# Kernel optimization log

Measured on AMD Instinct MI355X. Metric: run time of the kernel, lower is better.

## Reference

```python
import jax, jax.numpy as jnp
import numpy as np

N = 100000          # nodes
E = 1600000         # edges (before self-loops)
F_IN = 256          # num_node_features
F_MID = F_IN // 2   # conv1 out = 128
HID = 128           # hidden_channels
OUT = 64            # num_label_features
G = 128             # num graphs in batch
NEG_SLOPE = 0.2


def setup_inputs() -> dict:
    key = jax.random.key(0)
    ks = jax.random.split(key, 16)
    s = 0.05
    return {
        "x": jax.random.normal(ks[0], (N, F_IN), dtype=jnp.float32),
        "edge_index": jax.random.randint(ks[1], (2, E), 0, N, dtype=jnp.int64),
        "batch": jnp.sort(jax.random.randint(ks[2], (N,), 0, G, dtype=jnp.int64)),
        # GATConv 1 (heads=1)
        "W1": jax.random.normal(ks[3], (F_IN, F_MID), jnp.float32) * s,
        "a1_src": jax.random.normal(ks[4], (F_MID,), jnp.float32) * s,
        "a1_dst": jax.random.normal(ks[5], (F_MID,), jnp.float32) * s,
        "b1": jnp.zeros((F_MID,), jnp.float32),
        # GATConv 2
        "W2": jax.random.normal(ks[6], (F_MID, HID), jnp.float32) * s,
        "a2_src": jax.random.normal(ks[7], (HID,), jnp.float32) * s,
        "a2_dst": jax.random.normal(ks[8], (HID,), jnp.float32) * s,
        "b2": jnp.zeros((HID,), jnp.float32),
        # GlobalAttention gate nn
        "gate_W": jax.random.normal(ks[9], (HID, 1), jnp.float32) * s,
        "gate_b": jnp.zeros((1,), jnp.float32),
        # final linear
        "lin_W": jax.random.normal(ks[10], (HID, OUT), jnp.float32) * s,
        "lin_b": jnp.zeros((OUT,), jnp.float32),
    }


def _gat_conv(x, edge_index, W, a_src, a_dst, bias):
    """PyG GATConv, heads=1, add_self_loops=True, negative_slope=0.2."""
    n = x.shape[0]
    h = x @ W                                   # [N, F]
    loop = jnp.arange(n, dtype=edge_index.dtype)
    src = jnp.concatenate([edge_index[0], loop])  # message sources j
    dst = jnp.concatenate([edge_index[1], loop])  # aggregation targets i
    # per-node attention logits, gathered per-edge
    al = (h @ a_src)[src] + (h @ a_dst)[dst]    # [E+N]
    al = jax.nn.leaky_relu(al, NEG_SLOPE)
    # segment softmax over incoming edges of each dst node
    m = jax.ops.segment_max(al, dst, num_segments=n)
    e = jnp.exp(al - m[dst])
    s = jax.ops.segment_sum(e, dst, num_segments=n)
    coef = e / (s[dst] + 1e-16)
    out = jax.ops.segment_sum(h[src] * coef[:, None], dst, num_segments=n)
    return out + bias


def reference(x, edge_index, batch, W1, a1_src, a1_dst, b1,
              W2, a2_src, a2_dst, b2, gate_W, gate_b, lin_W, lin_b):
    h = _gat_conv(x, edge_index, W1, a1_src, a1_dst, b1)
    h = jax.nn.relu(h)
    h = _gat_conv(h, edge_index, W2, a2_src, a2_dst, b2)
    # GlobalAttention pooling: segment softmax of gate over batch ids
    gate = (h @ gate_W + gate_b)[:, 0]          # [N]
    gm = jax.ops.segment_max(gate, batch, num_segments=G)
    ge = jnp.exp(gate - gm[batch])
    gs = jax.ops.segment_sum(ge, batch, num_segments=G)
    attn = ge / (gs[batch] + 1e-16)
    pooled = jax.ops.segment_sum(h * attn[:, None], batch, num_segments=G)  # [G, HID]
    pooled = jax.nn.relu(pooled)
    # dropout p=0.5 is identity at inference
    return pooled @ lin_W + lin_b               # [G, OUT]
```

## Files before the change

### kernel.cpp

```cpp
#include <hip/hip_runtime.h>
#include <hip/hip_bf16.h>
#include <math.h>

#define NNODES 100000
#define NEDGES 1600000
#define EN     1700000
#define F_IN   256
#define F_MID  128
#define HID    128
#define NG     128
#define NOUT   64
#define SCAN_CHUNK 2048
#define NCHUNK ((NNODES + SCAN_CHUNK - 1) / SCAN_CHUNK)

typedef unsigned int  u32;
typedef unsigned short u16;

__device__ __forceinline__ float bfl(u32 u) { return __uint_as_float(u << 16); }
__device__ __forceinline__ float bfh(u32 u) { return __uint_as_float(u & 0xFFFF0000u); }
__device__ __forceinline__ u32 f2bf(float f) {
    u32 x = __float_as_uint(f);
    return (x + 0x7FFFu + ((x >> 16) & 1u)) >> 16;
}

__global__ __launch_bounds__(256) void k_init(int* deg, float* gs, float* pooled) {
    int i = blockIdx.x * 256 + threadIdx.x;
    if (i < NNODES) deg[i] = 1;
    if (i < NG) gs[i] = 0.f;
    if (i < NG * HID) pooled[i] = 0.f;
}

__global__ __launch_bounds__(256) void k_count(const int* __restrict__ ei, int* deg) {
    int e = blockIdx.x * 256 + threadIdx.x;
    if (e >= NEDGES) return;
    atomicAdd(&deg[ei[NEDGES + e]], 1);
}

__global__ __launch_bounds__(256) void k_scan_chunk(const int* __restrict__ deg,
                                                    int* rowptr, int* part) {
    __shared__ int sums[256];
    int c = blockIdx.x, t = threadIdx.x;
    int base = c * SCAN_CHUNK;
    int v[8]; int s = 0;
#pragma unroll
    for (int i = 0; i < 8; i++) {
        int idx = base + t * 8 + i;
        v[i] = (idx < NNODES) ? deg[idx] : 0;
        s += v[i];
    }
    sums[t] = s;
    __syncthreads();
    for (int off = 1; off < 256; off <<= 1) {
        int x = (t >= off) ? sums[t - off] : 0;
        __syncthreads();
        sums[t] += x;
        __syncthreads();
    }
    int run = (t == 0) ? 0 : sums[t - 1];
#pragma unroll
    for (int i = 0; i < 8; i++) {
        int idx = base + t * 8 + i;
        if (idx < NNODES) rowptr[idx] = run;
        run += v[i];
    }
    if (t == 255) part[c] = sums[255];
}

__global__ void k_scan_part(int* part, int nc) {
    if (threadIdx.x == 0) {
        int run = 0;
        for (int c = 0; c < nc; c++) { int v = part[c]; part[c] = run; run += v; }
    }
}

__global__ __launch_bounds__(256) void k_scan_add(int* rowptr, int* cursor,
                                                  const int* __restrict__ part) {
    int i = blockIdx.x * 256 + threadIdx.x;
    if (i >= NNODES) return;
    int v = rowptr[i] + part[i >> 11];
    rowptr[i] = v;
    cursor[i] = v;
}

__global__ __launch_bounds__(256) void k_fill(const int* __restrict__ ei,
                                              int* cursor, int* srcs) {
    int e = blockIdx.x * 256 + threadIdx.x;
    if (e >= EN) return;
    int src, dst;
    if (e < NEDGES) { src = ei[e]; dst = ei[NEDGES + e]; }
    else            { src = dst = e - NEDGES; }
    int pos = atomicAdd(&cursor[dst], 1);
    srcs[pos] = src;
}

template <int K, bool ABF>
__global__ __launch_bounds__(256) void k_gemm(const void* __restrict__ Av,
                                              const float* __restrict__ B,
                                              u16* __restrict__ C, int M) {
    __shared__ float As[16][128];
    __shared__ float Bs[16][128];
    int bm = blockIdx.x * 128;
    int tid = threadIdx.x;
    int tx = tid & 15, ty = tid >> 4;
    float acc[8][8] = {};
    for (int k0 = 0; k0 < K; k0 += 16) {
#pragma unroll
        for (int q = tid; q < 512; q += 256) {
            int m = q >> 2, kq = (q & 3) << 2;
            int row = bm + m;
            if (ABF) {
                const u16* A = (const u16*)Av;
                uint2 v = make_uint2(0u, 0u);
                if (row < M) v = *(const uint2*)(A + (size_t)row * K + k0 + kq);
                As[kq + 0][m] = bfl(v.x); As[kq + 1][m] = bfh(v.x);
                As[kq + 2][m] = bfl(v.y); As[kq + 3][m] = bfh(v.y);
            } else {
                const float* A = (const float*)Av;
                float4 v = make_float4(0.f, 0.f, 0.f, 0.f);
                if (row < M) v = *(const float4*)(A + (size_t)row * K + k0 + kq);
                As[kq + 0][m] = v.x; As[kq + 1][m] = v.y;
                As[kq + 2][m] = v.z; As[kq + 3][m] = v.w;
            }
        }
#pragma unroll
        for (int q = tid; q < 512; q += 256) {
            int kk = q >> 5, n4 = (q & 31) << 2;
            *(float4*)(&Bs[kk][n4]) = *(const float4*)(B + (size_t)(k0 + kk) * 128 + n4);
        }
        __syncthreads();
#pragma unroll
        for (int kk = 0; kk < 16; kk++) {
            float a[8], b[8];
            *(float4*)(a)     = *(float4*)(&As[kk][ty * 8]);
            *(float4*)(a + 4) = *(float4*)(&As[kk][ty * 8 + 4]);
            *(float4*)(b)     = *(float4*)(&Bs[kk][tx * 8]);
            *(float4*)(b + 4) = *(float4*)(&Bs[kk][tx * 8 + 4]);
#pragma unroll
            for (int i = 0; i < 8; i++)
#pragma unroll
                for (int j = 0; j < 8; j++)
                    acc[i][j] = fmaf(a[i], b[j], acc[i][j]);
        }
        __syncthreads();
    }
#pragma unroll
    for (int i = 0; i < 8; i++) {
        int row = bm + ty * 8 + i;
        if (row < M) {
            uint4 o;
            o.x = f2bf(acc[i][0]) | (f2bf(acc[i][1]) << 16);
            o.y = f2bf(acc[i][2]) | (f2bf(acc[i][3]) << 16);
            o.z = f2bf(acc[i][4]) | (f2bf(acc[i][5]) << 16);
            o.w = f2bf(acc[i][6]) | (f2bf(acc[i][7]) << 16);
            *(uint4*)(C + (size_t)row * 128 + tx * 8) = o;
        }
    }
}

__global__ __launch_bounds__(256) void k_dots(const u32* __restrict__ h,
                                              const float* __restrict__ asrc,
                                              const float* __restrict__ adst,
                                              float* as_, float* ad_) {
    int wid = (blockIdx.x * 256 + threadIdx.x) >> 6;
    int lane = threadIdx.x & 63;
    if (wid >= NNODES) return;
    u32 u = h[(size_t)wid * 64 + lane];
    float vx = bfl(u), vy = bfh(u);
    float2 as2 = ((const float2*)asrc)[lane];
    float2 ad2 = ((const float2*)adst)[lane];
    float s = vx * as2.x + vy * as2.y;
    float d = vx * ad2.x + vy * ad2.y;
#pragma unroll
    for (int off = 32; off; off >>= 1) {
        s += __shfl_xor(s, off);
        d += __shfl_xor(d, off);
    }
    if (lane == 0) { as_[wid] = s; ad_[wid] = d; }
}

template <bool RELU, bool GATE, bool OUTBF>
__global__ __launch_bounds__(256) void k_agg(
    const u32* __restrict__ h, const float* __restrict__ as_,
    const float* __restrict__ ad_, const int* __restrict__ rowptr,
    const int* __restrict__ rowend, const int* __restrict__ srcs,
    const float* __restrict__ bias, void* __restrict__ outv,
    const float* __restrict__ gateW, const float* __restrict__ gateB,
    float* __restrict__ gatev, float* __restrict__ gs,
    const int* __restrict__ batch) {
    int wid = (blockIdx.x * 256 + threadIdx.x) >> 6;
    int lane = threadIdx.x & 63;
    if (wid >= NNODES) return;
    int row = rowptr[wid];
    int dg = rowend[wid] - row;
    float adn = ad_[wid];

    float ssum = 0.f;
    float2 a0 = {0.f, 0.f}, a1 = {0.f, 0.f}, a2 = {0.f, 0.f}, a3 = {0.f, 0.f};
    float2 a4 = {0.f, 0.f}, a5 = {0.f, 0.f}, a6 = {0.f, 0.f}, a7 = {0.f, 0.f};

    for (int base = 0; base < dg; base += 64) {
        int k = base + lane;
        float ev = 0.f; int sk = 0;
        if (k < dg) {
            sk = srcs[row + k];
            float al = as_[sk] + adn;
            al = (al > 0.f) ? al : 0.2f * al;
            ev = __expf(al);
            ssum += ev;
        }
        int rem = dg - base; if (rem > 64) rem = 64;
        int kk = 0;
        for (; kk + 8 <= rem; kk += 8) {
            int   s0 = __shfl(sk, kk + 0), s1 = __shfl(sk, kk + 1);
            int   s2 = __shfl(sk, kk + 2), s3 = __shfl(sk, kk + 3);
            int   s4 = __shfl(sk, kk + 4), s5 = __shfl(sk, kk + 5);
            int   s6 = __shfl(sk, kk + 6), s7 = __shfl(sk, kk + 7);
            float e0 = __shfl(ev, kk + 0), e1 = __shfl(ev, kk + 1);
            float e2 = __shfl(ev, kk + 2), e3 = __shfl(ev, kk + 3);
            float e4 = __shfl(ev, kk + 4), e5 = __shfl(ev, kk + 5);
            float e6 = __shfl(ev, kk + 6), e7 = __shfl(ev, kk + 7);
            u32 u0 = h[(size_t)s0 * 64 + lane];
            u32 u1 = h[(size_t)s1 * 64 + lane];
            u32 u2 = h[(size_t)s2 * 64 + lane];
            u32 u3 = h[(size_t)s3 * 64 + lane];
            u32 u4 = h[(size_t)s4 * 64 + lane];
            u32 u5 = h[(size_t)s5 * 64 + lane];
            u32 u6 = h[(size_t)s6 * 64 + lane];
            u32 u7 = h[(size_t)s7 * 64 + lane];
            a0.x = fmaf(e0, bfl(u0), a0.x); a0.y = fmaf(e0, bfh(u0), a0.y);
            a1.x = fmaf(e1, bfl(u1), a1.x); a1.y = fmaf(e1, bfh(u1), a1.y);
            a2.x = fmaf(e2, bfl(u2), a2.x); a2.y = fmaf(e2, bfh(u2), a2.y);
            a3.x = fmaf(e3, bfl(u3), a3.x); a3.y = fmaf(e3, bfh(u3), a3.y);
            a4.x = fmaf(e4, bfl(u4), a4.x); a4.y = fmaf(e4, bfh(u4), a4.y);
            a5.x = fmaf(e5, bfl(u5), a5.x); a5.y = fmaf(e5, bfh(u5), a5.y);
            a6.x = fmaf(e6, bfl(u6), a6.x); a6.y = fmaf(e6, bfh(u6), a6.y);
            a7.x = fmaf(e7, bfl(u7), a7.x); a7.y = fmaf(e7, bfh(u7), a7.y);
        }
        for (; kk + 2 <= rem; kk += 2) {
            int   s0 = __shfl(sk, kk + 0), s1 = __shfl(sk, kk + 1);
            float e0 = __shfl(ev, kk + 0), e1 = __shfl(ev, kk + 1);
            u32 u0 = h[(size_t)s0 * 64 + lane];
            u32 u1 = h[(size_t)s1 * 64 + lane];
            a0.x = fmaf(e0, bfl(u0), a0.x); a0.y = fmaf(e0, bfh(u0), a0.y);
            a1.x = fmaf(e1, bfl(u1), a1.x); a1.y = fmaf(e1, bfh(u1), a1.y);
        }
        if (kk < rem) {
            int   s0 = __shfl(sk, kk);
            float e0 = __shfl(ev, kk);
            u32 u0 = h[(size_t)s0 * 64 + lane];
            a0.x = fmaf(e0, bfl(u0), a0.x); a0.y = fmaf(e0, bfh(u0), a0.y);
        }
    }
    float2 acc;
    acc.x = ((a0.x + a1.x) + (a2.x + a3.x)) + ((a4.x + a5.x) + (a6.x + a7.x));
    acc.y = ((a0.y + a1.y) + (a2.y + a3.y)) + ((a4.y + a5.y) + (a6.y + a7.y));
#pragma unroll
    for (int off = 32; off; off >>= 1) ssum += __shfl_xor(ssum, off);
    float inv = 1.f / (ssum + 1e-16f);
    float2 b2v = ((const float2*)bias)[lane];
    float o0 = acc.x * inv + b2v.x;
    float o1 = acc.y * inv + b2v.y;
    if (RELU) { o0 = fmaxf(o0, 0.f); o1 = fmaxf(o1, 0.f); }
    if (OUTBF) {
        ((u32*)outv)[(size_t)wid * 64 + lane] = f2bf(o0) | (f2bf(o1) << 16);
    } else {
        ((float2*)((float*)outv + (size_t)wid * 128))[lane] = make_float2(o0, o1);
    }
    if (GATE) {
        float2 gw = ((const float2*)gateW)[lane];
        float g = o0 * gw.x + o1 * gw.y;
#pragma unroll
        for (int off = 32; off; off >>= 1) g += __shfl_xor(g, off);
        if (lane == 0) {
            float ge = __expf(g + gateB[0]);
            gatev[wid] = ge;
            atomicAdd(&gs[batch[wid]], ge);
        }
    }
}

__global__ __launch_bounds__(128) void k_pool(const float* __restrict__ h,
                                              const float* __restrict__ gatev,
                                              const float* __restrict__ gs,
                                              const int* __restrict__ batch,
                                              float* pooled) {
    int t = threadIdx.x;
    int chunk = (NNODES + gridDim.x - 1) / gridDim.x;
    int s0 = blockIdx.x * chunk;
    int s1 = s0 + chunk; if (s1 > NNODES) s1 = NNODES;
    if (s0 >= s1) return;
    int curg = batch[s0];
    float invs = 1.f / (gs[curg] + 1e-16f);
    float acc = 0.f;
    for (int i = s0; i < s1; i++) {
        int g = batch[i];
        if (g != curg) {
            atomicAdd(&pooled[curg * 128 + t], acc);
            acc = 0.f; curg = g;
            invs = 1.f / (gs[g] + 1e-16f);
        }
        acc += h[(size_t)i * 128 + t] * (gatev[i] * invs);
    }
    atomicAdd(&pooled[curg * 128 + t], acc);
}

__global__ __launch_bounds__(64) void k_final(const float* __restrict__ pooled,
                                              const float* __restrict__ linW,
                                              const float* __restrict__ linb,
                                              float* __restrict__ out) {
    __shared__ float rowv[128];
    int g = blockIdx.x, t = threadIdx.x;
    rowv[t]      = fmaxf(pooled[g * 128 + t], 0.f);
    rowv[t + 64] = fmaxf(pooled[g * 128 + 64 + t], 0.f);
    __syncthreads();
    float acc = linb[t];
#pragma unroll 8
    for (int k = 0; k < 128; k++) acc = fmaf(rowv[k], linW[k * 64 + t], acc);
    out[g * 64 + t] = acc;
}

extern "C" void kernel_launch(void* const* d_in, const int* in_sizes, int n_in,
                              void* d_out, int out_size, void* d_ws, size_t ws_size,
                              hipStream_t stream) {
    const float* x     = (const float*)d_in[0];
    const int*   ei    = (const int*)d_in[1];
    const int*   batch = (const int*)d_in[2];
    const float* W1    = (const float*)d_in[3];
    const float* a1s   = (const float*)d_in[4];
    const float* a1d   = (const float*)d_in[5];
    const float* b1    = (const float*)d_in[6];
    const float* W2    = (const float*)d_in[7];
    const float* a2s   = (const float*)d_in[8];
    const float* a2d   = (const float*)d_in[9];
    const float* b2    = (const float*)d_in[10];
    const float* gateW = (const float*)d_in[11];
    const float* gateB = (const float*)d_in[12];
    const float* linW  = (const float*)d_in[13];
    const float* linb  = (const float*)d_in[14];
    float* out = (float*)d_out;

    char* p = (char*)d_ws;
    auto alloc = [&](size_t bytes) -> void* {
        void* r = (void*)p;
        p += (bytes + 255) & ~(size_t)255;
        return r;
    };
    u16*   hb     = (u16*)alloc((size_t)NNODES * 128 * 2);
    u16*   h1a    = (u16*)alloc((size_t)NNODES * 128 * 2);
    float* bufF   = (float*)alloc((size_t)NNODES * 128 * 4);
    float* as_    = (float*)alloc((size_t)NNODES * 4);
    float* ad_    = (float*)alloc((size_t)NNODES * 4);
    float* gatev  = (float*)alloc((size_t)NNODES * 4);
    int*   deg    = (int*)alloc((size_t)NNODES * 4);
    int*   rowptr = (int*)alloc((size_t)NNODES * 4);
    int*   cursor = (int*)alloc((size_t)NNODES * 4);
    int*   srcs   = (int*)alloc((size_t)EN * 4);
    int*   part   = (int*)alloc(64 * 4);
    float* gs     = (float*)alloc(NG * 4);
    float* pooled = (float*)alloc((size_t)NG * HID * 4);

    const int gN   = (NNODES + 255) / 256;
    const int gE   = (NEDGES + 255) / 256;
    const int gEN  = (EN + 255) / 256;
    const int gW   = (NNODES + 3) / 4;

    k_init<<<gN, 256, 0, stream>>>(deg, gs, pooled);
    k_count<<<gE, 256, 0, stream>>>(ei, deg);
    k_scan_chunk<<<NCHUNK, 256, 0, stream>>>(deg, rowptr, part);
    k_scan_part<<<1, 64, 0, stream>>>(part, NCHUNK);
    k_scan_add<<<gN, 256, 0, stream>>>(rowptr, cursor, part);
    k_fill<<<gEN, 256, 0, stream>>>(ei, cursor, srcs);

    k_gemm<256, false><<<(NNODES + 127) / 128, 256, 0, stream>>>(x, W1, hb, NNODES);
    k_dots<<<gW, 256, 0, stream>>>((const u32*)hb, a1s, a1d, as_, ad_);
    k_agg<true, false, true><<<gW, 256, 0, stream>>>((const u32*)hb, as_, ad_,
                                                     rowptr, cursor, srcs, b1, h1a,
                                                     nullptr, nullptr, nullptr,
                                                     nullptr, nullptr);
    k_gemm<128, true><<<(NNODES + 127) / 128, 256, 0, stream>>>(h1a, W2, hb, NNODES);
    k_dots<<<gW, 256, 0, stream>>>((const u32*)hb, a2s, a2d, as_, ad_);
    k_agg<false, true, false><<<gW, 256, 0, stream>>>((const u32*)hb, as_, ad_,
                                                      rowptr, cursor, srcs, b2, bufF,
                                                      gateW, gateB, gatev, gs, batch);
    k_pool<<<512, 128, 0, stream>>>(bufF, gatev, gs, batch, pooled);
    k_final<<<NG, 64, 0, stream>>>(pooled, linW, linb, out);
}
```

Before: 1.141 ms.

## Precompute packed per-edge source and exp-coefficient array before aggregation

A new k_coef kernel runs after each k_dots. It computes the leaky-relu/exp attention weight for every CSR edge and stores it next to the source index as an int2, using a new dsts array that k_fill now writes. k_agg then streams this packed meta array with wide vector loads, with no per-lane gathers of as_, no shuffles and no cross-lane reduction of ssum. It also gets a launch_bounds occupancy hint. The cost is an extra edge-sized kernel per layer plus extra memory traffic for dsts and meta. The int4 loads on int2-aligned addresses depend on unaligned access support.

```diff
diff --git a/kernel.cpp b/kernel.cpp
--- a/kernel.cpp
+++ b/kernel.cpp
@@ -83,7 +83,7 @@
 }
 
 __global__ __launch_bounds__(256) void k_fill(const int* __restrict__ ei,
-                                              int* cursor, int* srcs) {
+                                              int* cursor, int* srcs, int* dsts) {
     int e = blockIdx.x * 256 + threadIdx.x;
     if (e >= EN) return;
     int src, dst;
@@ -91,6 +91,21 @@
     else            { src = dst = e - NEDGES; }
     int pos = atomicAdd(&cursor[dst], 1);
     srcs[pos] = src;
+    dsts[pos] = dst;
+}
+
+__global__ __launch_bounds__(256) void k_coef(const int* __restrict__ srcs,
+                                              const int* __restrict__ dsts,
+                                              const float* __restrict__ as_,
+                                              const float* __restrict__ ad_,
+                                              int2* __restrict__ meta) {
+    int e = blockIdx.x * 256 + threadIdx.x;
+    if (e >= EN) return;
+    int s = srcs[e], d = dsts[e];
+    float al = as_[s] + ad_[d];
+    al = (al > 0.f) ? al : 0.2f * al;
+    float ev = __expf(al);
+    meta[e] = make_int2(s, __float_as_int(ev));
 }
 
 template <int K, bool ABF>
@@ -179,10 +194,9 @@
 }
 
 template <bool RELU, bool GATE, bool OUTBF>
-__global__ __launch_bounds__(256) void k_agg(
-    const u32* __restrict__ h, const float* __restrict__ as_,
-    const float* __restrict__ ad_, const int* __restrict__ rowptr,
-    const int* __restrict__ rowend, const int* __restrict__ srcs,
+__global__ __launch_bounds__(256, 4) void k_agg(
+    const u32* __restrict__ h, const int2* __restrict__ meta,
+    const int* __restrict__ rowptr, const int* __restrict__ rowend,
     const float* __restrict__ bias, void* __restrict__ outv,
     const float* __restrict__ gateW, const float* __restrict__ gateB,
     float* __restrict__ gatev, float* __restrict__ gs,
@@ -192,70 +206,76 @@
     if (wid >= NNODES) return;
     int row = rowptr[wid];
     int dg = rowend[wid] - row;
-    float adn = ad_[wid];
+    const int2* mp = meta + row;
 
     float ssum = 0.f;
     float2 a0 = {0.f, 0.f}, a1 = {0.f, 0.f}, a2 = {0.f, 0.f}, a3 = {0.f, 0.f};
-    float2 a4 = {0.f, 0.f}, a5 = {0.f, 0.f}, a6 = {0.f, 0.f}, a7 = {0.f, 0.f};
-
-    for (int base = 0; base < dg; base += 64) {
-        int k = base + lane;
-        float ev = 0.f; int sk = 0;
-        if (k < dg) {
-            sk = srcs[row + k];
-            float al = as_[sk] + adn;
-            al = (al > 0.f) ? al : 0.2f * al;
-            ev = __expf(al);
-            ssum += ev;
-        }
-        int rem = dg - base; if (rem > 64) rem = 64;
-        int kk = 0;
-        for (; kk + 8 <= rem; kk += 8) {
-            int   s0 = __shfl(sk, kk + 0), s1 = __shfl(sk, kk + 1);
-            int   s2 = __shfl(sk, kk + 2), s3 = __shfl(sk, kk + 3);
-            int   s4 = __shfl(sk, kk + 4), s5 = __shfl(sk, kk + 5);
-            int   s6 = __shfl(sk, kk + 6), s7 = __shfl(sk, kk + 7);
-            float e0 = __shfl(ev, kk + 0), e1 = __shfl(ev, kk + 1);
-            float e2 = __shfl(ev, kk + 2), e3 = __shfl(ev, kk + 3);
-            float e4 = __shfl(ev, kk + 4), e5 = __shfl(ev, kk + 5);
-            float e6 = __shfl(ev, kk + 6), e7 = __shfl(ev, kk + 7);
-            u32 u0 = h[(size_t)s0 * 64 + lane];
-            u32 u1 = h[(size_t)s1 * 64 + lane];
-            u32 u2 = h[(size_t)s2 * 64 + lane];
-            u32 u3 = h[(size_t)s3 * 64 + lane];
-            u32 u4 = h[(size_t)s4 * 64 + lane];
-            u32 u5 = h[(size_t)s5 * 64 + lane];
-            u32 u6 = h[(size_t)s6 * 64 + lane];
-            u32 u7 = h[(size_t)s7 * 64 + lane];
-            a0.x = fmaf(e0, bfl(u0), a0.x); a0.y = fmaf(e0, bfh(u0), a0.y);
-            a1.x = fmaf(e1, bfl(u1), a1.x); a1.y = fmaf(e1, bfh(u1), a1.y);
-            a2.x = fmaf(e2, bfl(u2), a2.x); a2.y = fmaf(e2, bfh(u2), a2.y);
-            a3.x = fmaf(e3, bfl(u3), a3.x); a3.y = fmaf(e3, bfh(u3), a3.y);
-            a4.x = fmaf(e4, bfl(u4), a4.x); a4.y = fmaf(e4, bfh(u4), a4.y);
-            a5.x = fmaf(e5, bfl(u5), a5.x); a5.y = fmaf(e5, bfh(u5), a5.y);
-            a6.x = fmaf(e6, bfl(u6), a6.x); a6.y = fmaf(e6, bfh(u6), a6.y);
-            a7.x = fmaf(e7, bfl(u7), a7.x); a7.y = fmaf(e7, bfh(u7), a7.y);
-        }
-        for (; kk + 2 <= rem; kk += 2) {
-            int   s0 = __shfl(sk, kk + 0), s1 = __shfl(sk, kk + 1);
-            float e0 = __shfl(ev, kk + 0), e1 = __shfl(ev, kk + 1);
-            u32 u0 = h[(size_t)s0 * 64 + lane];
-            u32 u1 = h[(size_t)s1 * 64 + lane];
-            a0.x = fmaf(e0, bfl(u0), a0.x); a0.y = fmaf(e0, bfh(u0), a0.y);
-            a1.x = fmaf(e1, bfl(u1), a1.x); a1.y = fmaf(e1, bfh(u1), a1.y);
-        }
-        if (kk < rem) {
-            int   s0 = __shfl(sk, kk);
-            float e0 = __shfl(ev, kk);
-            u32 u0 = h[(size_t)s0 * 64 + lane];
-            a0.x = fmaf(e0, bfl(u0), a0.x); a0.y = fmaf(e0, bfh(u0), a0.y);
-        }
-    }
+
+    int i = 0;
+    for (; i + 8 <= dg; i += 8) {
+        int4 ma = *(const int4*)(mp + i);
+        int4 mb = *(const int4*)(mp + i + 2);
+        int4 mc = *(const int4*)(mp + i + 4);
+        int4 md = *(const int4*)(mp + i + 6);
+        u32 u0 = h[(size_t)ma.x * 64 + lane];
+        u32 u1 = h[(size_t)ma.z * 64 + lane];
+        u32 u2 = h[(size_t)mb.x * 64 + lane];
+        u32 u3 = h[(size_t)mb.z * 64 + lane];
+        u32 u4 = h[(size_t)mc.x * 64 + lane];
+        u32 u5 = h[(size_t)mc.z * 64 + lane];
+        u32 u6 = h[(size_t)md.x * 64 + lane];
+        u32 u7 = h[(size_t)md.z * 64 + lane];
+        float e0 = __int_as_float(ma.y), e1 = __int_as_float(ma.w);
+        float e2 = __int_as_float(mb.y), e3 = __int_as_float(mb.w);
+        float e4 = __int_as_float(mc.y), e5 = __int_as_float(mc.w);
+        float e6 = __int_as_float(md.y), e7 = __int_as_float(md.w);
+        ssum += ((e0 + e1) + (e2 + e3)) + ((e4 + e5) + (e6 + e7));
+        a0.x = fmaf(e0, bfl(u0), a0.x); a0.y = fmaf(e0, bfh(u0), a0.y);
+        a1.x = fmaf(e1, bfl(u1), a1.x); a1.y = fmaf(e1, bfh(u1), a1.y);
+        a2.x = fmaf(e2, bfl(u2), a2.x); a2.y = fmaf(e2, bfh(u2), a2.y);
+        a3.x = fmaf(e3, bfl(u3), a3.x); a3.y = fmaf(e3, bfh(u3), a3.y);
+        a0.x = fmaf(e4, bfl(u4), a0.x); a0.y = fmaf(e4, bfh(u4), a0.y);
+        a1.x = fmaf(e5, bfl(u5), a1.x); a1.y = fmaf(e5, bfh(u5), a1.y);
+        a2.x = fmaf(e6, bfl(u6), a2.x); a2.y = fmaf(e6, bfh(u6), a2.y);
+        a3.x = fmaf(e7, bfl(u7), a3.x); a3.y = fmaf(e7, bfh(u7), a3.y);
+    }
+    if (i + 4 <= dg) {
+        int4 ma = *(const int4*)(mp + i);
+        int4 mb = *(const int4*)(mp + i + 2);
+        u32 u0 = h[(size_t)ma.x * 64 + lane];
+        u32 u1 = h[(size_t)ma.z * 64 + lane];
+        u32 u2 = h[(size_t)mb.x * 64 + lane];
+        u32 u3 = h[(size_t)mb.z * 64 + lane];
+        float e0 = __int_as_float(ma.y), e1 = __int_as_float(ma.w);
+        float e2 = __int_as_float(mb.y), e3 = __int_as_float(mb.w);
+        ssum += (e0 + e1) + (e2 + e3);
+        a0.x = fmaf(e0, bfl(u0), a0.x); a0.y = fmaf(e0, bfh(u0), a0.y);
+        a1.x = fmaf(e1, bfl(u1), a1.x); a1.y = fmaf(e1, bfh(u1), a1.y);
+        a2.x = fmaf(e2, bfl(u2), a2.x); a2.y = fmaf(e2, bfh(u2), a2.y);
+        a3.x = fmaf(e3, bfl(u3), a3.x); a3.y = fmaf(e3, bfh(u3), a3.y);
+        i += 4;
+    }
+    if (i + 2 <= dg) {
+        int4 ma = *(const int4*)(mp + i);
+        u32 u0 = h[(size_t)ma.x * 64 + lane];
+        u32 u1 = h[(size_t)ma.z * 64 + lane];
+        float e0 = __int_as_float(ma.y), e1 = __int_as_float(ma.w);
+        ssum += e0 + e1;
+        a0.x = fmaf(e0, bfl(u0), a0.x); a0.y = fmaf(e0, bfh(u0), a0.y);
+        a1.x = fmaf(e1, bfl(u1), a1.x); a1.y = fmaf(e1, bfh(u1), a1.y);
+        i += 2;
+    }
+    if (i < dg) {
+        int2 m = mp[i];
+        u32 u0 = h[(size_t)m.x * 64 + lane];
+        float e0 = __int_as_float(m.y);
+        ssum += e0;
+        a0.x = fmaf(e0, bfl(u0), a0.x); a0.y = fmaf(e0, bfh(u0), a0.y);
+    }
+
     float2 acc;
-    acc.x = ((a0.x + a1.x) + (a2.x + a3.x)) + ((a4.x + a5.x) + (a6.x + a7.x));
-    acc.y = ((a0.y + a1.y) + (a2.y + a3.y)) + ((a4.y + a5.y) + (a6.y + a7.y));
-#pragma unroll
-    for (int off = 32; off; off >>= 1) ssum += __shfl_xor(ssum, off);
+    acc.x = (a0.x + a1.x) + (a2.x + a3.x);
+    acc.y = (a0.y + a1.y) + (a2.y + a3.y);
     float inv = 1.f / (ssum + 1e-16f);
     float2 b2v = ((const float2*)bias)[lane];
     float o0 = acc.x * inv + b2v.x;
@@ -355,6 +375,8 @@
     int*   rowptr = (int*)alloc((size_t)NNODES * 4);
     int*   cursor = (int*)alloc((size_t)NNODES * 4);
     int*   srcs   = (int*)alloc((size_t)EN * 4);
+    int*   dsts   = (int*)alloc((size_t)EN * 4);
+    int2*  meta   = (int2*)alloc((size_t)EN * 8);
     int*   part   = (int*)alloc(64 * 4);
     float* gs     = (float*)alloc(NG * 4);
     float* pooled = (float*)alloc((size_t)NG * HID * 4);
@@ -369,18 +391,20 @@
     k_scan_chunk<<<NCHUNK, 256, 0, stream>>>(deg, rowptr, part);
     k_scan_part<<<1, 64, 0, stream>>>(part, NCHUNK);
     k_scan_add<<<gN, 256, 0, stream>>>(rowptr, cursor, part);
-    k_fill<<<gEN, 256, 0, stream>>>(ei, cursor, srcs);
+    k_fill<<<gEN, 256, 0, stream>>>(ei, cursor, srcs, dsts);
 
     k_gemm<256, false><<<(NNODES + 127) / 128, 256, 0, stream>>>(x, W1, hb, NNODES);
     k_dots<<<gW, 256, 0, stream>>>((const u32*)hb, a1s, a1d, as_, ad_);
-    k_agg<true, false, true><<<gW, 256, 0, stream>>>((const u32*)hb, as_, ad_,
-                                                     rowptr, cursor, srcs, b1, h1a,
+    k_coef<<<gEN, 256, 0, stream>>>(srcs, dsts, as_, ad_, meta);
+    k_agg<true, false, true><<<gW, 256, 0, stream>>>((const u32*)hb, meta,
+                                                     rowptr, cursor, b1, h1a,
                                                      nullptr, nullptr, nullptr,
                                                      nullptr, nullptr);
     k_gemm<128, true><<<(NNODES + 127) / 128, 256, 0, stream>>>(h1a, W2, hb, NNODES);
     k_dots<<<gW, 256, 0, stream>>>((const u32*)hb, a2s, a2d, as_, ad_);
-    k_agg<false, true, false><<<gW, 256, 0, stream>>>((const u32*)hb, as_, ad_,
-                                                      rowptr, cursor, srcs, b2, bufF,
+    k_coef<<<gEN, 256, 0, stream>>>(srcs, dsts, as_, ad_, meta);
+    k_agg<false, true, false><<<gW, 256, 0, stream>>>((const u32*)hb, meta,
+                                                      rowptr, cursor, b2, bufF,
                                                       gateW, gateB, gatev, gs, batch);
     k_pool<<<512, 128, 0, stream>>>(bufF, gatev, gs, batch, pooled);
     k_final<<<NG, 64, 0, stream>>>(pooled, linW, linb, out);
```

Result: slower. 1.222 ms (+7.1%).

## Precompute edge attention weights and stage neighbor rows via global-to-LDS loads

Applied to the files above, without the earlier changes.

The CSR fill now stores (src,dst) pairs, and a new per-edge kernel computes the leaky-ReLU and exp attention weight for each edge ahead of aggregation, writing (src, weight) pairs. The aggregation kernel drops the per-lane logit computation and wave shuffles. It instead reads the packed pairs in chunks of 8 and pulls neighbor feature rows directly into LDS with global_load_lds, waiting on vmcnt before accumulating. This targets shuffle and ALU overhead in the gather loop, but adds two extra edge-sized passes. It also pads every node's degree up to a multiple of 8 and fully drains loads after each chunk, which may reduce how much memory latency is hidden.

```diff
diff --git a/kernel.cpp b/kernel.cpp
--- a/kernel.cpp
+++ b/kernel.cpp
@@ -12,6 +12,7 @@
 #define NOUT   64
 #define SCAN_CHUNK 2048
 #define NCHUNK ((NNODES + SCAN_CHUNK - 1) / SCAN_CHUNK)
+#define CHUNK  8
 
 typedef unsigned int  u32;
 typedef unsigned short u16;
@@ -21,6 +22,13 @@
 __device__ __forceinline__ u32 f2bf(float f) {
     u32 x = __float_as_uint(f);
     return (x + 0x7FFFu + ((x >> 16) & 1u)) >> 16;
+}
+
+__device__ __forceinline__ void gload_lds4(const u32* g, u32* ldsbase) {
+    __builtin_amdgcn_global_load_lds(
+        (const __attribute__((address_space(1))) u32*)(uintptr_t)g,
+        (__attribute__((address_space(3))) u32*)(u32)(uintptr_t)ldsbase,
+        4, 0, 0);
 }
 
 __global__ __launch_bounds__(256) void k_init(int* deg, float* gs, float* pooled) {
@@ -83,14 +91,26 @@
 }
 
 __global__ __launch_bounds__(256) void k_fill(const int* __restrict__ ei,
-                                              int* cursor, int* srcs) {
+                                              int* cursor, int2* meta0) {
     int e = blockIdx.x * 256 + threadIdx.x;
     if (e >= EN) return;
     int src, dst;
     if (e < NEDGES) { src = ei[e]; dst = ei[NEDGES + e]; }
     else            { src = dst = e - NEDGES; }
     int pos = atomicAdd(&cursor[dst], 1);
-    srcs[pos] = src;
+    meta0[pos] = make_int2(src, dst);
+}
+
+__global__ __launch_bounds__(256) void k_coef(const int2* __restrict__ meta0,
+                                              const float* __restrict__ as_,
+                                              const float* __restrict__ ad_,
+                                              int2* __restrict__ meta1) {
+    int e = blockIdx.x * 256 + threadIdx.x;
+    if (e >= EN) return;
+    int2 sd = meta0[e];
+    float al = as_[sd.x] + ad_[sd.y];
+    al = (al > 0.f) ? al : 0.2f * al;
+    meta1[e] = make_int2(sd.x, __float_as_int(__expf(al)));
 }
 
 template <int K, bool ABF>
@@ -180,86 +200,49 @@
 
 template <bool RELU, bool GATE, bool OUTBF>
 __global__ __launch_bounds__(256) void k_agg(
-    const u32* __restrict__ h, const float* __restrict__ as_,
-    const float* __restrict__ ad_, const int* __restrict__ rowptr,
-    const int* __restrict__ rowend, const int* __restrict__ srcs,
+    const u32* __restrict__ h, const int2* __restrict__ meta,
+    const int* __restrict__ rowptr, const int* __restrict__ rowend,
     const float* __restrict__ bias, void* __restrict__ outv,
     const float* __restrict__ gateW, const float* __restrict__ gateB,
     float* __restrict__ gatev, float* __restrict__ gs,
     const int* __restrict__ batch) {
-    int wid = (blockIdx.x * 256 + threadIdx.x) >> 6;
-    int lane = threadIdx.x & 63;
+    __shared__ u32 lbuf[4][CHUNK * 64];
+    int tid = threadIdx.x;
+    int w = tid >> 6, lane = tid & 63;
+    int wid = blockIdx.x * 4 + w;
     if (wid >= NNODES) return;
     int row = rowptr[wid];
     int dg = rowend[wid] - row;
-    float adn = ad_[wid];
-
-    float ssum = 0.f;
-    float2 a0 = {0.f, 0.f}, a1 = {0.f, 0.f}, a2 = {0.f, 0.f}, a3 = {0.f, 0.f};
-    float2 a4 = {0.f, 0.f}, a5 = {0.f, 0.f}, a6 = {0.f, 0.f}, a7 = {0.f, 0.f};
-
-    for (int base = 0; base < dg; base += 64) {
-        int k = base + lane;
-        float ev = 0.f; int sk = 0;
-        if (k < dg) {
-            sk = srcs[row + k];
-            float al = as_[sk] + adn;
-            al = (al > 0.f) ? al : 0.2f * al;
-            ev = __expf(al);
+    const int2* mp = meta + row;
+    u32* wb = &lbuf[w][0];
+
+    float ssum = 0.f, ax = 0.f, ay = 0.f;
+    for (int cb = 0; cb < dg; cb += CHUNK) {
+        asm volatile("s_waitcnt lgkmcnt(0)" ::: "memory");
+        int2 mm[CHUNK];
+#pragma unroll
+        for (int j = 0; j < CHUNK; j++) {
+            int idx = cb + j;
+            mm[j] = mp[(idx < dg) ? idx : dg - 1];
+        }
+#pragma unroll
+        for (int j = 0; j < CHUNK; j++)
+            gload_lds4(h + (size_t)mm[j].x * 64 + lane, wb + j * 64);
+        asm volatile("s_waitcnt vmcnt(0)" ::: "memory");
+#pragma unroll
+        for (int j = 0; j < CHUNK; j++) {
+            float ev = ((cb + j) < dg) ? __int_as_float(mm[j].y) : 0.f;
+            u32 u = wb[j * 64 + lane];
             ssum += ev;
-        }
-        int rem = dg - base; if (rem > 64) rem = 64;
-        int kk = 0;
-        for (; kk + 8 <= rem; kk += 8) {
-            int   s0 = __shfl(sk, kk + 0), s1 = __shfl(sk, kk + 1);
-            int   s2 = __shfl(sk, kk + 2), s3 = __shfl(sk, kk + 3);
-            int   s4 = __shfl(sk, kk + 4), s5 = __shfl(sk, kk + 5);
-            int   s6 = __shfl(sk, kk + 6), s7 = __shfl(sk, kk + 7);
-            float e0 = __shfl(ev, kk + 0), e1 = __shfl(ev, kk + 1);
-            float e2 = __shfl(ev, kk + 2), e3 = __shfl(ev, kk + 3);
-            float e4 = __shfl(ev, kk + 4), e5 = __shfl(ev, kk + 5);
-            float e6 = __shfl(ev, kk + 6), e7 = __shfl(ev, kk + 7);
-            u32 u0 = h[(size_t)s0 * 64 + lane];
-            u32 u1 = h[(size_t)s1 * 64 + lane];
-            u32 u2 = h[(size_t)s2 * 64 + lane];
-            u32 u3 = h[(size_t)s3 * 64 + lane];
-            u32 u4 = h[(size_t)s4 * 64 + lane];
-            u32 u5 = h[(size_t)s5 * 64 + lane];
-            u32 u6 = h[(size_t)s6 * 64 + lane];
-            u32 u7 = h[(size_t)s7 * 64 + lane];
-            a0.x = fmaf(e0, bfl(u0), a0.x); a0.y = fmaf(e0, bfh(u0), a0.y);
-            a1.x = fmaf(e1, bfl(u1), a1.x); a1.y = fmaf(e1, bfh(u1), a1.y);
-            a2.x = fmaf(e2, bfl(u2), a2.x); a2.y = fmaf(e2, bfh(u2), a2.y);
-            a3.x = fmaf(e3, bfl(u3), a3.x); a3.y = fmaf(e3, bfh(u3), a3.y);
-            a4.x = fmaf(e4, bfl(u4), a4.x); a4.y = fmaf(e4, bfh(u4), a4.y);
-            a5.x = fmaf(e5, bfl(u5), a5.x); a5.y = fmaf(e5, bfh(u5), a5.y);
-            a6.x = fmaf(e6, bfl(u6), a6.x); a6.y = fmaf(e6, bfh(u6), a6.y);
-            a7.x = fmaf(e7, bfl(u7), a7.x); a7.y = fmaf(e7, bfh(u7), a7.y);
-        }
-        for (; kk + 2 <= rem; kk += 2) {
-            int   s0 = __shfl(sk, kk + 0), s1 = __shfl(sk, kk + 1);
-            float e0 = __shfl(ev, kk + 0), e1 = __shfl(ev, kk + 1);
-            u32 u0 = h[(size_t)s0 * 64 + lane];
-            u32 u1 = h[(size_t)s1 * 64 + lane];
-            a0.x = fmaf(e0, bfl(u0), a0.x); a0.y = fmaf(e0, bfh(u0), a0.y);
-            a1.x = fmaf(e1, bfl(u1), a1.x); a1.y = fmaf(e1, bfh(u1), a1.y);
-        }
-        if (kk < rem) {
-            int   s0 = __shfl(sk, kk);
-            float e0 = __shfl(ev, kk);
-            u32 u0 = h[(size_t)s0 * 64 + lane];
-            a0.x = fmaf(e0, bfl(u0), a0.x); a0.y = fmaf(e0, bfh(u0), a0.y);
-        }
-    }
-    float2 acc;
-    acc.x = ((a0.x + a1.x) + (a2.x + a3.x)) + ((a4.x + a5.x) + (a6.x + a7.x));
-    acc.y = ((a0.y + a1.y) + (a2.y + a3.y)) + ((a4.y + a5.y) + (a6.y + a7.y));
-#pragma unroll
-    for (int off = 32; off; off >>= 1) ssum += __shfl_xor(ssum, off);
+            ax = fmaf(ev, bfl(u), ax);
+            ay = fmaf(ev, bfh(u), ay);
+        }
+    }
+
     float inv = 1.f / (ssum + 1e-16f);
     float2 b2v = ((const float2*)bias)[lane];
-    float o0 = acc.x * inv + b2v.x;
-    float o1 = acc.y * inv + b2v.y;
+    float o0 = ax * inv + b2v.x;
+    float o1 = ay * inv + b2v.y;
     if (RELU) { o0 = fmaxf(o0, 0.f); o1 = fmaxf(o1, 0.f); }
     if (OUTBF) {
         ((u32*)outv)[(size_t)wid * 64 + lane] = f2bf(o0) | (f2bf(o1) << 16);
@@ -346,15 +329,17 @@
         return r;
     };
     u16*   hb     = (u16*)alloc((size_t)NNODES * 128 * 2);
-    u16*   h1a    = (u16*)alloc((size_t)NNODES * 128 * 2);
-    float* bufF   = (float*)alloc((size_t)NNODES * 128 * 4);
+    char*  region = (char*)alloc((size_t)NNODES * 128 * 4);
+    u16*   h1a    = (u16*)region;
+    int2*  meta0  = (int2*)(region + (size_t)NNODES * 128 * 2);
+    float* bufF   = (float*)region;
+    int2*  meta1  = (int2*)alloc((size_t)EN * 8);
     float* as_    = (float*)alloc((size_t)NNODES * 4);
     float* ad_    = (float*)alloc((size_t)NNODES * 4);
     float* gatev  = (float*)alloc((size_t)NNODES * 4);
     int*   deg    = (int*)alloc((size_t)NNODES * 4);
     int*   rowptr = (int*)alloc((size_t)NNODES * 4);
     int*   cursor = (int*)alloc((size_t)NNODES * 4);
-    int*   srcs   = (int*)alloc((size_t)EN * 4);
     int*   part   = (int*)alloc(64 * 4);
     float* gs     = (float*)alloc(NG * 4);
     float* pooled = (float*)alloc((size_t)NG * HID * 4);
@@ -369,18 +354,20 @@
     k_scan_chunk<<<NCHUNK, 256, 0, stream>>>(deg, rowptr, part);
     k_scan_part<<<1, 64, 0, stream>>>(part, NCHUNK);
     k_scan_add<<<gN, 256, 0, stream>>>(rowptr, cursor, part);
-    k_fill<<<gEN, 256, 0, stream>>>(ei, cursor, srcs);
+    k_fill<<<gEN, 256, 0, stream>>>(ei, cursor, meta0);
 
     k_gemm<256, false><<<(NNODES + 127) / 128, 256, 0, stream>>>(x, W1, hb, NNODES);
     k_dots<<<gW, 256, 0, stream>>>((const u32*)hb, a1s, a1d, as_, ad_);
-    k_agg<true, false, true><<<gW, 256, 0, stream>>>((const u32*)hb, as_, ad_,
-                                                     rowptr, cursor, srcs, b1, h1a,
+    k_coef<<<gEN, 256, 0, stream>>>(meta0, as_, ad_, meta1);
+    k_agg<true, false, true><<<gW, 256, 0, stream>>>((const u32*)hb, meta1,
+                                                     rowptr, cursor, b1, h1a,
                                                      nullptr, nullptr, nullptr,
                                                      nullptr, nullptr);
     k_gemm<128, true><<<(NNODES + 127) / 128, 256, 0, stream>>>(h1a, W2, hb, NNODES);
     k_dots<<<gW, 256, 0, stream>>>((const u32*)hb, a2s, a2d, as_, ad_);
-    k_agg<false, true, false><<<gW, 256, 0, stream>>>((const u32*)hb, as_, ad_,
-                                                      rowptr, cursor, srcs, b2, bufF,
+    k_coef<<<gEN, 256, 0, stream>>>(meta0, as_, ad_, meta1);
+    k_agg<false, true, false><<<gW, 256, 0, stream>>>((const u32*)hb, meta1,
+                                                      rowptr, cursor, b2, bufF,
                                                       gateW, gateB, gatev, gs, batch);
     k_pool<<<512, 128, 0, stream>>>(bufF, gatev, gs, batch, pooled);
     k_final<<<NG, 64, 0, stream>>>(pooled, linW, linb, out);
```

New measurement: 1.217 ms. 6.6% more time.
